# Kernel tuning notes

Measured on AMD Instinct MI355X. Metric: run time of the kernel, lower is better.

The kernel has to match this reference:

```python
import jax, jax.numpy as jnp
import numpy as np

B, L, E, H, D = 4, 4096, 1024, 16, 64  # batch, seq, embed, heads, head_dim
EPS = 1e-6


def setup_inputs() -> dict:
    key = jax.random.key(0)
    k1, k2, k3 = jax.random.split(key, 3)
    return {
        "q": jax.random.normal(k1, (B, L, E), dtype=jnp.float32),
        "k": jax.random.normal(k2, (B, L, E), dtype=jnp.float32),
        "v": jax.random.normal(k3, (B, L, E), dtype=jnp.float32),
        "mask": jnp.ones((B, L), dtype=jnp.float32),
    }


def _split_heads(x):
    # (B, L, E) -> (B*H, L, D)
    return x.reshape(B, L, H, D).transpose(0, 2, 1, 3).reshape(B * H, L, D)


def reference(q, k, v, mask):
    # feature map: relu
    q = jax.nn.relu(q)
    k = jax.nn.relu(k)
    # padding mask applied to keys/values
    k = k * mask[:, :, None]
    v = v * mask[:, :, None]
    q = _split_heads(q)
    k = _split_heads(k)
    v = _split_heads(v)
    # cosFormer sin/cos reweighting: pi/2 * i / m for i = 1..L
    idx = (np.pi / 2) * jnp.arange(1, L + 1, dtype=jnp.float32) / L
    s = jnp.sin(idx)[None, :, None]  # (1, L, 1)
    c = jnp.cos(idx)[None, :, None]
    q_ = jnp.concatenate([q * s, q * c], axis=-1)  # (B*H, L, 2D)
    k_ = jnp.concatenate([k * s, k * c], axis=-1)
    # linear-attention KV accumulation (non-causal): (B*H, 2D, D)
    kv = jnp.einsum('nld,nlm->ndm', k_, v)
    # normalizer
    z = 1.0 / jnp.maximum(jnp.einsum('nld,nd->nl', q_, k_.sum(axis=1)), EPS)
    out = jnp.einsum('nld,ndm,nl->nlm', q_, kv, z)  # (B*H, L, D)
    return out.reshape(B, H, L, D)
```

## Files before the change

### kernel.cpp

```cpp
#include <hip/hip_runtime.h>
#include <hip/hip_bf16.h>

#define B_ 4
#define L_ 4096
#define E_ 1024
#define H_ 16
#define D_ 64
#define N_ 64
#define D2_ 128
#define EPS_ 1e-6f

#define CH_ 16
#define LC_ 256
#define ANGSC (0.5f * 3.14159265358979f / (float)L_)

typedef short short8 __attribute__((ext_vector_type(8)));
typedef float f32x4 __attribute__((ext_vector_type(4)));
typedef unsigned int u32;
typedef unsigned short u16;

static __device__ __forceinline__ u16 bf16u(float x) {
  union { __hip_bfloat16 h; u16 s; } u;
  u.h = __float2bfloat16(x);
  return u.s;
}
static __device__ __forceinline__ u32 pack2bf(float a, float b) {
  return (u32)bf16u(a) | ((u32)bf16u(b) << 16);
}

__global__ __launch_bounds__(256, 4) void phase1_mfma(
    const float* __restrict__ k, const float* __restrict__ v,
    const float* __restrict__ mask,
    float* __restrict__ part_kv, float* __restrict__ part_ks) {
  __shared__ __align__(16) u16 ka[D2_ * 72];
  __shared__ __align__(16) u16 vt[D_ * 72];
  __shared__ float mm[LC_], ms[LC_], mc[LC_];

  const int bid = blockIdx.x;
  const int n = bid & 63, ch = bid >> 6;
  const int b = n >> 4, h = n & 15;
  const int t = threadIdx.x;
  const int wv = t >> 6, lane = t & 63;
  const int c_lo = lane & 15, lp = lane >> 4;
  const int c = wv * 16 + c_lo;

  {
    const int gl = ch * LC_ + t;
    const float m = mask[b * L_ + gl];
    const float ang = (float)(gl + 1) * ANGSC;
    mm[t] = m;
    ms[t] = m * __sinf(ang);
    mc[t] = m * __cosf(ang);
  }

  const float* kbase = k + (size_t)(b * L_ + ch * LC_) * E_ + h * 64 + c;
  const float* vbase = v + (size_t)(b * L_ + ch * LC_) * E_ + h * 64 + c;

  float pk0[8], pk1[8], pv0[8], pv1[8];
#pragma unroll
  for (int i = 0; i < 8; ++i) {
    const int l = 8 * i + 2 * lp;
    pk0[i] = kbase[(size_t)l * E_];
    pk1[i] = kbase[(size_t)(l + 1) * E_];
    pv0[i] = vbase[(size_t)l * E_];
    pv1[i] = vbase[(size_t)(l + 1) * E_];
  }

  f32x4 acc[2][4];
#pragma unroll
  for (int i = 0; i < 2; ++i)
#pragma unroll
    for (int j = 0; j < 4; ++j) acc[i][j] = (f32x4)0.f;
  float kss = 0.f, ksc = 0.f;

  for (int st = 0; st < 4; ++st) {
    __syncthreads();
#pragma unroll
    for (int i = 0; i < 8; ++i) {
      const int l = 8 * i + 2 * lp, lg = st * 64 + l, li = 4 * i + lp;
      const float kr0 = fmaxf(pk0[i], 0.f), kr1 = fmaxf(pk1[i], 0.f);
      const float a0 = kr0 * ms[lg], a1 = kr1 * ms[lg + 1];
      const float c0 = kr0 * mc[lg], c1 = kr1 * mc[lg + 1];
      ((u32*)ka)[c * 36 + li] = pack2bf(a0, a1);
      ((u32*)ka)[(c + 64) * 36 + li] = pack2bf(c0, c1);
      ((u32*)vt)[c * 36 + li] = pack2bf(pv0[i] * mm[lg], pv1[i] * mm[lg + 1]);
      kss += a0 + a1;
      ksc += c0 + c1;
    }
    __syncthreads();
    if (st < 3) {
      const int lo = (st + 1) * 64;
#pragma unroll
      for (int i = 0; i < 8; ++i) {
        const int l = lo + 8 * i + 2 * lp;
        pk0[i] = kbase[(size_t)l * E_];
        pk1[i] = kbase[(size_t)(l + 1) * E_];
        pv0[i] = vbase[(size_t)l * E_];
        pv1[i] = vbase[(size_t)(l + 1) * E_];
      }
    }
#pragma unroll
    for (int kk = 0; kk < 2; ++kk) {
      const int colo = kk * 32 + lp * 8;
      short8 af[2], bfr[4];
#pragma unroll
      for (int dt = 0; dt < 2; ++dt)
        af[dt] = *(const short8*)&ka[(wv * 32 + dt * 16 + c_lo) * 72 + colo];
#pragma unroll
      for (int mt = 0; mt < 4; ++mt)
        bfr[mt] = *(const short8*)&vt[(mt * 16 + c_lo) * 72 + colo];
#pragma unroll
      for (int dt = 0; dt < 2; ++dt)
#pragma unroll
        for (int mt = 0; mt < 4; ++mt)
          acc[dt][mt] = __builtin_amdgcn_mfma_f32_16x16x32_bf16(
              af[dt], bfr[mt], acc[dt][mt], 0, 0, 0);
    }
  }

  const size_t pbase = (size_t)(ch * N_ + n) * (D2_ * D_);
#pragma unroll
  for (int dt = 0; dt < 2; ++dt) {
    const int d = wv * 32 + dt * 16 + lp * 4;
#pragma unroll
    for (int mt = 0; mt < 4; ++mt) {
      const int mcol = mt * 16 + c_lo;
#pragma unroll
      for (int r = 0; r < 4; ++r)
        part_kv[pbase + (size_t)(d + r) * D_ + mcol] = acc[dt][mt][r];
    }
  }
  kss += __shfl_xor(kss, 16); kss += __shfl_xor(kss, 32);
  ksc += __shfl_xor(ksc, 16); ksc += __shfl_xor(ksc, 32);
  if (lp == 0) {
    part_ks[(size_t)(ch * N_ + n) * D2_ + c] = kss;
    part_ks[(size_t)(ch * N_ + n) * D2_ + c + 64] = ksc;
  }
}

__global__ __launch_bounds__(256) void reduce_t(
    const float* __restrict__ part_kv, const float* __restrict__ part_ks,
    u16* __restrict__ kvt, u16* __restrict__ ksb) {
  __shared__ float l0[8][65], l1[8][65];
  const int n = blockIdx.x & 63, fs = blockIdx.x >> 6;
  const int t = threadIdx.x;

#pragma unroll
  for (int p = 0; p < 4; ++p) {
    const int idx = t + 256 * p;
    const int g = idx >> 9, dd = (idx >> 6) & 7, m = idx & 63;
    const int d = g * 64 + fs * 8 + dd;
    float s = 0.f;
#pragma unroll
    for (int cc = 0; cc < CH_; ++cc)
      s += part_kv[(size_t)(cc * N_ + n) * (D2_ * D_) + d * 64 + m];
    if (g == 0) l0[dd][m] = s; else l1[dd][m] = s;
  }
  if (fs == 0 && t < D2_) {
    float s = 0.f;
#pragma unroll
    for (int cc = 0; cc < CH_; ++cc)
      s += part_ks[(size_t)(cc * N_ + n) * D2_ + t];
    const int dloc = t & 63, half = t >> 6;
    ksb[n * D2_ + 2 * dloc + half] = bf16u(s);
  }
  __syncthreads();
  u32* kvt32 = (u32*)(kvt + (size_t)n * (D_ * D2_));
#pragma unroll
  for (int p = 0; p < 2; ++p) {
    const int idx = t + 256 * p;
    const int j = idx & 7, m = idx >> 3;
    kvt32[m * 64 + fs * 8 + j] = pack2bf(l0[j][m], l1[j][m]);
  }
}

__global__ __launch_bounds__(256, 4) void phase2_mfma(
    const float* __restrict__ q, const u16* __restrict__ kvt,
    const u16* __restrict__ ksb, float* __restrict__ out) {
  const int bid = blockIdx.x;
  const int n = bid & 63, lt = bid >> 6;
  const int b = n >> 4, h = n & 15;
  const int t = threadIdx.x;
  const int wv = t >> 6, lane = t & 63;
  const int c_lo = lane & 15, quad = lane >> 4;
  const int l = lt * 64 + wv * 16 + c_lo;

  const float ang = (float)(l + 1) * ANGSC;
  const float sn = __sinf(ang), cs = __cosf(ang);

  const float* qrow = q + (size_t)(b * L_ + l) * E_ + h * 64;
  short8 af[4];
#pragma unroll
  for (int kk = 0; kk < 4; ++kk) {
    const float4 qv = *(const float4*)(qrow + kk * 16 + quad * 4);
    const float x = fmaxf(qv.x, 0.f), y = fmaxf(qv.y, 0.f);
    const float z2 = fmaxf(qv.z, 0.f), w = fmaxf(qv.w, 0.f);
    short8 a;
    a[0] = (short)bf16u(x * sn); a[1] = (short)bf16u(x * cs);
    a[2] = (short)bf16u(y * sn); a[3] = (short)bf16u(y * cs);
    a[4] = (short)bf16u(z2 * sn); a[5] = (short)bf16u(z2 * cs);
    a[6] = (short)bf16u(w * sn); a[7] = (short)bf16u(w * cs);
    af[kk] = a;
  }

  const u16* kvh = kvt + (size_t)n * (D_ * D2_);
  const u16* ksh = ksb + n * D2_;
  f32x4 acc[4], acc5 = (f32x4)0.f;
#pragma unroll
  for (int mt = 0; mt < 4; ++mt) acc[mt] = (f32x4)0.f;

#pragma unroll
  for (int kk = 0; kk < 4; ++kk) {
    const int fo = kk * 32 + quad * 8;
#pragma unroll
    for (int mt = 0; mt < 4; ++mt) {
      const short8 bfr = *(const short8*)&kvh[(mt * 16 + c_lo) * D2_ + fo];
      acc[mt] = __builtin_amdgcn_mfma_f32_16x16x32_bf16(af[kk], bfr, acc[mt], 0, 0, 0);
    }
    const short8 bks = *(const short8*)&ksh[fo];
    acc5 = __builtin_amdgcn_mfma_f32_16x16x32_bf16(af[kk], bks, acc5, 0, 0, 0);
  }

#pragma unroll
  for (int r = 0; r < 4; ++r) {
    const float den = __shfl(acc5[r], quad * 16);
    const float zz = 1.f / fmaxf(den, EPS_);
    const int gl = lt * 64 + wv * 16 + quad * 4 + r;
    float* ob = out + (size_t)n * (L_ * D_) + (size_t)gl * D_;
#pragma unroll
    for (int mt = 0; mt < 4; ++mt) ob[mt * 16 + c_lo] = acc[mt][r] * zz;
  }
}

extern "C" void kernel_launch(void* const* d_in, const int* in_sizes, int n_in,
                              void* d_out, int out_size, void* d_ws,
                              size_t ws_size, hipStream_t stream) {
  const float* q = (const float*)d_in[0];
  const float* k = (const float*)d_in[1];
  const float* v = (const float*)d_in[2];
  const float* mask = (const float*)d_in[3];
  float* out = (float*)d_out;

  float* part_kv = (float*)d_ws;
  float* part_ks = part_kv + (size_t)CH_ * N_ * D2_ * D_;
  u16* kvt = (u16*)(part_ks + (size_t)CH_ * N_ * D2_);
  u16* ksb = kvt + (size_t)N_ * D2_ * D_;

  phase1_mfma<<<dim3(CH_ * N_), dim3(256), 0, stream>>>(k, v, mask, part_kv, part_ks);
  reduce_t<<<dim3(8 * N_), dim3(256), 0, stream>>>(part_kv, part_ks, kvt, ksb);
  phase2_mfma<<<dim3(N_ * 64), dim3(256), 0, stream>>>(q, kvt, ksb, out);
}
```

Before: 266.1 us.

## Pre-transpose K/V/Q into bf16 head-major layouts before MFMA phases

Adds transpose kernels that read K, V and Q with coalesced row loads and write bf16, head-major, MFMA-friendly tiles. The sin/cos weights are moved from K onto V, and the key-sum is computed via MFMA against sin/cos tables. A single-block-per-head reduction replaces the strided reduce. The goal is to remove uncoalesced strided fp32 loads in the phase kernels, at the cost of extra launches and roughly 100MB of extra intermediate global traffic. If the workspace is too small, the old path is used instead.

```diff
diff --git a/kernel.cpp b/kernel.cpp
--- a/kernel.cpp
+++ b/kernel.cpp
@@ -9,9 +9,7 @@
 #define N_ 64
 #define D2_ 128
 #define EPS_ 1e-6f
-
 #define CH_ 16
-#define LC_ 256
 #define ANGSC (0.5f * 3.14159265358979f / (float)L_)
 
 typedef short short8 __attribute__((ext_vector_type(8)));
@@ -28,14 +26,256 @@
   return (u32)bf16u(a) | ((u32)bf16u(b) << 16);
 }
 
-__global__ __launch_bounds__(256, 4) void phase1_mfma(
+
+__global__ __launch_bounds__(256, 2) void t_kv(
+    const float* __restrict__ k, const float* __restrict__ v,
+    const float* __restrict__ mask, u32* __restrict__ kt,
+    u32* __restrict__ vs, u32* __restrict__ vc,
+    u16* __restrict__ tabs_s, u16* __restrict__ tabs_c) {
+  __shared__ float sh[16][1028];
+  __shared__ float msk[16], mss[16], msc[16];
+
+  const int bid = blockIdx.x;
+  const int b = bid >> 8, lt = bid & 255;
+  const int l0 = lt * 16;
+  const int t = threadIdx.x;
+
+  if (t < 16) {
+    const int gl = l0 + t;
+    const float m = mask[b * L_ + gl];
+    const float ang = (float)(gl + 1) * ANGSC;
+    const float s = __sinf(ang), c = __cosf(ang);
+    msk[t] = m; mss[t] = m * s; msc[t] = m * c;
+    if (b == 0) { tabs_s[gl] = bf16u(s); tabs_c[gl] = bf16u(c); }
+  }
+  __syncthreads();
+
+  {
+    const float* kb = k + (size_t)(b * L_ + l0) * E_;
+#pragma unroll
+    for (int rr = 0; rr < 4; ++rr) {
+      const int row = (t >> 6) + rr * 4;
+#pragma unroll
+      for (int seg = 0; seg < 4; ++seg) {
+        const int c4 = (t & 63) + seg * 64;
+        *(float4*)&sh[row][c4 * 4] = *(const float4*)(kb + (size_t)row * E_ + c4 * 4);
+      }
+    }
+  }
+  __syncthreads();
+  {
+    const int d = t >> 2, lw = (t & 3) * 2;
+#pragma unroll
+    for (int h = 0; h < 16; ++h) {
+      const int c = h * 64 + d;
+      const int la = 2 * lw;
+      const float x0 = fmaxf(sh[la][c], 0.f) * msk[la];
+      const float x1 = fmaxf(sh[la + 1][c], 0.f) * msk[la + 1];
+      const float x2 = fmaxf(sh[la + 2][c], 0.f) * msk[la + 2];
+      const float x3 = fmaxf(sh[la + 3][c], 0.f) * msk[la + 3];
+      const size_t base = ((size_t)(b * 16 + h) * 256 + lt) * 512;
+      uint2 val = { pack2bf(x0, x1), pack2bf(x2, x3) };
+      *(uint2*)&kt[base + d * 8 + lw] = val;
+    }
+  }
+  __syncthreads();
+  {
+    const float* vb = v + (size_t)(b * L_ + l0) * E_;
+#pragma unroll
+    for (int rr = 0; rr < 4; ++rr) {
+      const int row = (t >> 6) + rr * 4;
+#pragma unroll
+      for (int seg = 0; seg < 4; ++seg) {
+        const int c4 = (t & 63) + seg * 64;
+        *(float4*)&sh[row][c4 * 4] = *(const float4*)(vb + (size_t)row * E_ + c4 * 4);
+      }
+    }
+  }
+  __syncthreads();
+  {
+    const int m = t >> 2, lw = (t & 3) * 2;
+#pragma unroll
+    for (int h = 0; h < 16; ++h) {
+      const int c = h * 64 + m;
+      const int la = 2 * lw;
+      const float y0 = sh[la][c], y1 = sh[la + 1][c];
+      const float y2 = sh[la + 2][c], y3 = sh[la + 3][c];
+      const size_t base = ((size_t)(b * 16 + h) * 256 + lt) * 512;
+      uint2 a = { pack2bf(y0 * mss[la], y1 * mss[la + 1]),
+                  pack2bf(y2 * mss[la + 2], y3 * mss[la + 3]) };
+      uint2 cc = { pack2bf(y0 * msc[la], y1 * msc[la + 1]),
+                   pack2bf(y2 * msc[la + 2], y3 * msc[la + 3]) };
+      *(uint2*)&vs[base + m * 8 + lw] = a;
+      *(uint2*)&vc[base + m * 8 + lw] = cc;
+    }
+  }
+}
+
+__global__ __launch_bounds__(256, 4) void t_q(
+    const float* __restrict__ q, u32* __restrict__ qo) {
+  const int bid = blockIdx.x;
+  const int b = bid >> 8, l0 = (bid & 255) * 16;
+  const int t = threadIdx.x;
+  const int h = t & 15, lr = t >> 4;
+  const int l = l0 + lr;
+
+  const float ang = (float)(l + 1) * ANGSC;
+  const float s = __sinf(ang), c = __cosf(ang);
+
+  const float* qrow = q + (size_t)(b * L_ + l) * E_ + h * 64;
+  u32* qout = qo + ((size_t)(b * 16 + h) * L_ + l) * 64;
+#pragma unroll
+  for (int i = 0; i < 16; ++i) {
+    const float4 qv = *(const float4*)(qrow + i * 4);
+    const float x = fmaxf(qv.x, 0.f), y = fmaxf(qv.y, 0.f);
+    const float zz = fmaxf(qv.z, 0.f), w = fmaxf(qv.w, 0.f);
+    uint4 o = { pack2bf(x * s, x * c), pack2bf(y * s, y * c),
+                pack2bf(zz * s, zz * c), pack2bf(w * s, w * c) };
+    *(uint4*)&qout[i * 4] = o;
+  }
+}
+
+__global__ __launch_bounds__(256, 4) void p1(
+    const u16* __restrict__ kt, const u16* __restrict__ vs,
+    const u16* __restrict__ vc, const u16* __restrict__ tabs_s,
+    const u16* __restrict__ tabs_c,
+    float* __restrict__ part_kv, float* __restrict__ part_ks) {
+  const int bid = blockIdx.x;
+  const int n = bid & 63, ch = bid >> 6;
+  const int t = threadIdx.x;
+  const int wv = t >> 6, lane = t & 63;
+  const int c_lo = lane & 15, quad = lane >> 4;
+
+  const u16* ktn = kt + (size_t)n * (256 * 1024);
+  const u16* vsn = vs + (size_t)n * (256 * 1024);
+  const u16* vcn = vc + (size_t)n * (256 * 1024);
+
+  f32x4 accE[4], accO[4], aS = (f32x4)0.f, aC = (f32x4)0.f;
+#pragma unroll
+  for (int i = 0; i < 4; ++i) { accE[i] = (f32x4)0.f; accO[i] = (f32x4)0.f; }
+
+  const int d = wv * 16 + c_lo;
+#pragma unroll
+  for (int ks = 0; ks < 8; ++ks) {
+    const int lg = ch * 256 + ks * 32 + quad * 8;
+    const int ltt = lg >> 4, lin = lg & 15;
+    const short8 af = *(const short8*)&ktn[((size_t)ltt * 64 + d) * 16 + lin];
+    const short8 bs = *(const short8*)&tabs_s[lg];
+    const short8 bc = *(const short8*)&tabs_c[lg];
+    aS = __builtin_amdgcn_mfma_f32_16x16x32_bf16(af, bs, aS, 0, 0, 0);
+    aC = __builtin_amdgcn_mfma_f32_16x16x32_bf16(af, bc, aC, 0, 0, 0);
+#pragma unroll
+    for (int mt = 0; mt < 4; ++mt) {
+      const int m = mt * 16 + c_lo;
+      const short8 bE = *(const short8*)&vsn[((size_t)ltt * 64 + m) * 16 + lin];
+      const short8 bO = *(const short8*)&vcn[((size_t)ltt * 64 + m) * 16 + lin];
+      accE[mt] = __builtin_amdgcn_mfma_f32_16x16x32_bf16(af, bE, accE[mt], 0, 0, 0);
+      accO[mt] = __builtin_amdgcn_mfma_f32_16x16x32_bf16(af, bO, accO[mt], 0, 0, 0);
+    }
+  }
+
+  float* pb = part_kv + ((size_t)(ch * 64 + n)) * (128 * 64);
+#pragma unroll
+  for (int r = 0; r < 4; ++r) {
+    const int dd = wv * 16 + quad * 4 + r;
+#pragma unroll
+    for (int mt = 0; mt < 4; ++mt) {
+      const int m = mt * 16 + c_lo;
+      pb[(size_t)(2 * dd) * 64 + m] = accE[mt][r];
+      pb[(size_t)(2 * dd + 1) * 64 + m] = accO[mt][r];
+    }
+    if (c_lo == 0) {
+      part_ks[((size_t)(ch * 64 + n)) * 128 + 2 * dd] = aS[r];
+      part_ks[((size_t)(ch * 64 + n)) * 128 + 2 * dd + 1] = aC[r];
+    }
+  }
+}
+
+__global__ __launch_bounds__(256) void reduce_k(
+    const float* __restrict__ part_kv, const float* __restrict__ part_ks,
+    u16* __restrict__ kvt, u16* __restrict__ ksb) {
+  __shared__ u16 kvsh[64 * 136];
+  const int n = blockIdx.x;
+  const int t = threadIdx.x;
+
+  float a[32];
+#pragma unroll
+  for (int j = 0; j < 32; ++j) a[j] = 0.f;
+#pragma unroll
+  for (int cc = 0; cc < CH_; ++cc) {
+    const float* p = part_kv + ((size_t)(cc * 64 + n)) * 8192 + t * 32;
+#pragma unroll
+    for (int j = 0; j < 8; ++j) {
+      const float4 x = *(const float4*)(p + j * 4);
+      a[4 * j] += x.x; a[4 * j + 1] += x.y; a[4 * j + 2] += x.z; a[4 * j + 3] += x.w;
+    }
+  }
+  if (t < 128) {
+    float s = 0.f;
+#pragma unroll
+    for (int cc = 0; cc < CH_; ++cc)
+      s += part_ks[((size_t)(cc * 64 + n)) * 128 + t];
+    ksb[n * 128 + t] = bf16u(s);
+  }
+  const int f = t >> 1, m0 = (t & 1) * 32;
+#pragma unroll
+  for (int j = 0; j < 32; ++j) kvsh[(m0 + j) * 136 + f] = bf16u(a[j]);
+  __syncthreads();
+  const int m = t >> 2, fo = (t & 3) * 32;
+  u16* o = kvt + (size_t)n * 8192 + m * 128 + fo;
+#pragma unroll
+  for (int j = 0; j < 4; ++j)
+    *(short8*)(o + j * 8) = *(short8*)&kvsh[m * 136 + fo + j * 8];
+}
+
+__global__ __launch_bounds__(256, 4) void p2(
+    const u16* __restrict__ qo, const u16* __restrict__ kvt,
+    const u16* __restrict__ ksb, float* __restrict__ out) {
+  const int bid = blockIdx.x;
+  const int n = bid & 63, lt = bid >> 6;
+  const int t = threadIdx.x;
+  const int wv = t >> 6, lane = t & 63;
+  const int c_lo = lane & 15, quad = lane >> 4;
+  const int l = lt * 64 + wv * 16 + c_lo;
+
+  const u16* qrow = qo + ((size_t)n * L_ + l) * 128;
+  const u16* kvh = kvt + (size_t)n * 8192;
+  const u16* ksh = ksb + n * 128;
+
+  f32x4 acc[4], acc5 = (f32x4)0.f;
+#pragma unroll
+  for (int mt = 0; mt < 4; ++mt) acc[mt] = (f32x4)0.f;
+
+#pragma unroll
+  for (int kk = 0; kk < 4; ++kk) {
+    const int fo = kk * 32 + quad * 8;
+    const short8 af = *(const short8*)&qrow[fo];
+#pragma unroll
+    for (int mt = 0; mt < 4; ++mt) {
+      const short8 bfr = *(const short8*)&kvh[(mt * 16 + c_lo) * 128 + fo];
+      acc[mt] = __builtin_amdgcn_mfma_f32_16x16x32_bf16(af, bfr, acc[mt], 0, 0, 0);
+    }
+    const short8 bks = *(const short8*)&ksh[fo];
+    acc5 = __builtin_amdgcn_mfma_f32_16x16x32_bf16(af, bks, acc5, 0, 0, 0);
+  }
+
+#pragma unroll
+  for (int r = 0; r < 4; ++r) {
+    const float zz = 1.f / fmaxf(acc5[r], EPS_);
+    const int gl = lt * 64 + wv * 16 + quad * 4 + r;
+    float* ob = out + (size_t)n * (L_ * D_) + (size_t)gl * D_;
+#pragma unroll
+    for (int mt = 0; mt < 4; ++mt) ob[mt * 16 + c_lo] = acc[mt][r] * zz;
+  }
+}
+
+__global__ __launch_bounds__(256, 4) void r3_phase1(
     const float* __restrict__ k, const float* __restrict__ v,
     const float* __restrict__ mask,
     float* __restrict__ part_kv, float* __restrict__ part_ks) {
   __shared__ __align__(16) u16 ka[D2_ * 72];
   __shared__ __align__(16) u16 vt[D_ * 72];
-  __shared__ float mm[LC_], ms[LC_], mc[LC_];
-
+  __shared__ float mm[256], ms[256], mc[256];
   const int bid = blockIdx.x;
   const int n = bid & 63, ch = bid >> 6;
   const int b = n >> 4, h = n & 15;
@@ -43,36 +283,27 @@
   const int wv = t >> 6, lane = t & 63;
   const int c_lo = lane & 15, lp = lane >> 4;
   const int c = wv * 16 + c_lo;
-
   {
-    const int gl = ch * LC_ + t;
+    const int gl = ch * 256 + t;
     const float m = mask[b * L_ + gl];
     const float ang = (float)(gl + 1) * ANGSC;
-    mm[t] = m;
-    ms[t] = m * __sinf(ang);
-    mc[t] = m * __cosf(ang);
-  }
-
-  const float* kbase = k + (size_t)(b * L_ + ch * LC_) * E_ + h * 64 + c;
-  const float* vbase = v + (size_t)(b * L_ + ch * LC_) * E_ + h * 64 + c;
-
+    mm[t] = m; ms[t] = m * __sinf(ang); mc[t] = m * __cosf(ang);
+  }
+  const float* kbase = k + (size_t)(b * L_ + ch * 256) * E_ + h * 64 + c;
+  const float* vbase = v + (size_t)(b * L_ + ch * 256) * E_ + h * 64 + c;
   float pk0[8], pk1[8], pv0[8], pv1[8];
 #pragma unroll
   for (int i = 0; i < 8; ++i) {
     const int l = 8 * i + 2 * lp;
-    pk0[i] = kbase[(size_t)l * E_];
-    pk1[i] = kbase[(size_t)(l + 1) * E_];
-    pv0[i] = vbase[(size_t)l * E_];
-    pv1[i] = vbase[(size_t)(l + 1) * E_];
-  }
-
+    pk0[i] = kbase[(size_t)l * E_]; pk1[i] = kbase[(size_t)(l + 1) * E_];
+    pv0[i] = vbase[(size_t)l * E_]; pv1[i] = vbase[(size_t)(l + 1) * E_];
+  }
   f32x4 acc[2][4];
 #pragma unroll
   for (int i = 0; i < 2; ++i)
 #pragma unroll
     for (int j = 0; j < 4; ++j) acc[i][j] = (f32x4)0.f;
   float kss = 0.f, ksc = 0.f;
-
   for (int st = 0; st < 4; ++st) {
     __syncthreads();
 #pragma unroll
@@ -84,8 +315,7 @@
       ((u32*)ka)[c * 36 + li] = pack2bf(a0, a1);
       ((u32*)ka)[(c + 64) * 36 + li] = pack2bf(c0, c1);
       ((u32*)vt)[c * 36 + li] = pack2bf(pv0[i] * mm[lg], pv1[i] * mm[lg + 1]);
-      kss += a0 + a1;
-      ksc += c0 + c1;
+      kss += a0 + a1; ksc += c0 + c1;
     }
     __syncthreads();
     if (st < 3) {
@@ -93,10 +323,8 @@
 #pragma unroll
       for (int i = 0; i < 8; ++i) {
         const int l = lo + 8 * i + 2 * lp;
-        pk0[i] = kbase[(size_t)l * E_];
-        pk1[i] = kbase[(size_t)(l + 1) * E_];
-        pv0[i] = vbase[(size_t)l * E_];
-        pv1[i] = vbase[(size_t)(l + 1) * E_];
+        pk0[i] = kbase[(size_t)l * E_]; pk1[i] = kbase[(size_t)(l + 1) * E_];
+        pv0[i] = vbase[(size_t)l * E_]; pv1[i] = vbase[(size_t)(l + 1) * E_];
       }
     }
 #pragma unroll
@@ -117,17 +345,16 @@
               af[dt], bfr[mt], acc[dt][mt], 0, 0, 0);
     }
   }
-
   const size_t pbase = (size_t)(ch * N_ + n) * (D2_ * D_);
 #pragma unroll
   for (int dt = 0; dt < 2; ++dt) {
-    const int d = wv * 32 + dt * 16 + lp * 4;
+    const int dd = wv * 32 + dt * 16 + lp * 4;
 #pragma unroll
     for (int mt = 0; mt < 4; ++mt) {
       const int mcol = mt * 16 + c_lo;
 #pragma unroll
       for (int r = 0; r < 4; ++r)
-        part_kv[pbase + (size_t)(d + r) * D_ + mcol] = acc[dt][mt][r];
+        part_kv[pbase + (size_t)(dd + r) * D_ + mcol] = acc[dt][mt][r];
     }
   }
   kss += __shfl_xor(kss, 16); kss += __shfl_xor(kss, 32);
@@ -138,13 +365,12 @@
   }
 }
 
-__global__ __launch_bounds__(256) void reduce_t(
+__global__ __launch_bounds__(256) void r3_reduce(
     const float* __restrict__ part_kv, const float* __restrict__ part_ks,
     u16* __restrict__ kvt, u16* __restrict__ ksb) {
-  __shared__ float l0[8][65], l1[8][65];
+  __shared__ float l0s[8][65], l1s[8][65];
   const int n = blockIdx.x & 63, fs = blockIdx.x >> 6;
   const int t = threadIdx.x;
-
 #pragma unroll
   for (int p = 0; p < 4; ++p) {
     const int idx = t + 256 * p;
@@ -154,15 +380,14 @@
 #pragma unroll
     for (int cc = 0; cc < CH_; ++cc)
       s += part_kv[(size_t)(cc * N_ + n) * (D2_ * D_) + d * 64 + m];
-    if (g == 0) l0[dd][m] = s; else l1[dd][m] = s;
+    if (g == 0) l0s[dd][m] = s; else l1s[dd][m] = s;
   }
   if (fs == 0 && t < D2_) {
     float s = 0.f;
 #pragma unroll
     for (int cc = 0; cc < CH_; ++cc)
       s += part_ks[(size_t)(cc * N_ + n) * D2_ + t];
-    const int dloc = t & 63, half = t >> 6;
-    ksb[n * D2_ + 2 * dloc + half] = bf16u(s);
+    ksb[n * D2_ + 2 * (t & 63) + (t >> 6)] = bf16u(s);
   }
   __syncthreads();
   u32* kvt32 = (u32*)(kvt + (size_t)n * (D_ * D2_));
@@ -170,11 +395,11 @@
   for (int p = 0; p < 2; ++p) {
     const int idx = t + 256 * p;
     const int j = idx & 7, m = idx >> 3;
-    kvt32[m * 64 + fs * 8 + j] = pack2bf(l0[j][m], l1[j][m]);
-  }
-}
-
-__global__ __launch_bounds__(256, 4) void phase2_mfma(
+    kvt32[m * 64 + fs * 8 + j] = pack2bf(l0s[j][m], l1s[j][m]);
+  }
+}
+
+__global__ __launch_bounds__(256, 4) void r3_phase2(
     const float* __restrict__ q, const u16* __restrict__ kvt,
     const u16* __restrict__ ksb, float* __restrict__ out) {
   const int bid = blockIdx.x;
@@ -184,10 +409,8 @@
   const int wv = t >> 6, lane = t & 63;
   const int c_lo = lane & 15, quad = lane >> 4;
   const int l = lt * 64 + wv * 16 + c_lo;
-
   const float ang = (float)(l + 1) * ANGSC;
   const float sn = __sinf(ang), cs = __cosf(ang);
-
   const float* qrow = q + (size_t)(b * L_ + l) * E_ + h * 64;
   short8 af[4];
 #pragma unroll
@@ -202,13 +425,11 @@
     a[6] = (short)bf16u(w * sn); a[7] = (short)bf16u(w * cs);
     af[kk] = a;
   }
-
   const u16* kvh = kvt + (size_t)n * (D_ * D2_);
   const u16* ksh = ksb + n * D2_;
   f32x4 acc[4], acc5 = (f32x4)0.f;
 #pragma unroll
   for (int mt = 0; mt < 4; ++mt) acc[mt] = (f32x4)0.f;
-
 #pragma unroll
   for (int kk = 0; kk < 4; ++kk) {
     const int fo = kk * 32 + quad * 8;
@@ -220,7 +441,6 @@
     const short8 bks = *(const short8*)&ksh[fo];
     acc5 = __builtin_amdgcn_mfma_f32_16x16x32_bf16(af[kk], bks, acc5, 0, 0, 0);
   }
-
 #pragma unroll
   for (int r = 0; r < 4; ++r) {
     const float den = __shfl(acc5[r], quad * 16);
@@ -240,13 +460,43 @@
   const float* v = (const float*)d_in[2];
   const float* mask = (const float*)d_in[3];
   float* out = (float*)d_out;
-
-  float* part_kv = (float*)d_ws;
-  float* part_ks = part_kv + (size_t)CH_ * N_ * D2_ * D_;
-  u16* kvt = (u16*)(part_ks + (size_t)CH_ * N_ * D2_);
-  u16* ksb = kvt + (size_t)N_ * D2_ * D_;
-
-  phase1_mfma<<<dim3(CH_ * N_), dim3(256), 0, stream>>>(k, v, mask, part_kv, part_ks);
-  reduce_t<<<dim3(8 * N_), dim3(256), 0, stream>>>(part_kv, part_ks, kvt, ksb);
-  phase2_mfma<<<dim3(N_ * 64), dim3(256), 0, stream>>>(q, kvt, ksb, out);
-}
+  char* ws = (char*)d_ws;
+
+  const size_t SZ_KT = 33554432, SZ_VS = 33554432, SZ_VC = 33554432;
+  const size_t SZ_PKV = 33554432, SZ_PKS = 524288, SZ_KVT = 1048576;
+  const size_t SZ_KSB = 16384, SZ_TAB = 16384;
+  const size_t o_kt = 0, o_vs = o_kt + SZ_KT, o_vc = o_vs + SZ_VS;
+  const size_t o_pkv = o_vc + SZ_VC, o_pks = o_pkv + SZ_PKV;
+  const size_t o_kvt = o_pks + SZ_PKS, o_ksb = o_kvt + SZ_KVT;
+  const size_t o_ts = o_ksb + SZ_KSB, o_tc = o_ts + SZ_TAB / 2;
+  const size_t need = o_tc + SZ_TAB / 2;
+
+  if (ws_size >= need) {
+    u32* kt = (u32*)(ws + o_kt);
+    u32* vs = (u32*)(ws + o_vs);
+    u32* vc = (u32*)(ws + o_vc);
+    float* part_kv = (float*)(ws + o_pkv);
+    float* part_ks = (float*)(ws + o_pks);
+    u16* kvt = (u16*)(ws + o_kvt);
+    u16* ksb = (u16*)(ws + o_ksb);
+    u16* tabs_s = (u16*)(ws + o_ts);
+    u16* tabs_c = (u16*)(ws + o_tc);
+    u32* qo = (u32*)(ws + o_kt);
+
+    t_kv<<<dim3(4 * 256), dim3(256), 0, stream>>>(k, v, mask, kt, vs, vc,
+                                                  tabs_s, tabs_c);
+    p1<<<dim3(CH_ * 64), dim3(256), 0, stream>>>((u16*)kt, (u16*)vs, (u16*)vc,
+                                                 tabs_s, tabs_c, part_kv, part_ks);
+    t_q<<<dim3(4 * 256), dim3(256), 0, stream>>>(q, qo);
+    reduce_k<<<dim3(64), dim3(256), 0, stream>>>(part_kv, part_ks, kvt, ksb);
+    p2<<<dim3(64 * 64), dim3(256), 0, stream>>>((u16*)qo, kvt, ksb, out);
+  } else {
+    float* part_kv = (float*)d_ws;
+    float* part_ks = part_kv + (size_t)CH_ * N_ * D2_ * D_;
+    u16* kvt = (u16*)(part_ks + (size_t)CH_ * N_ * D2_);
+    u16* ksb = kvt + (size_t)N_ * D2_ * D_;
+    r3_phase1<<<dim3(CH_ * N_), dim3(256), 0, stream>>>(k, v, mask, part_kv, part_ks);
+    r3_reduce<<<dim3(8 * N_), dim3(256), 0, stream>>>(part_kv, part_ks, kvt, ksb);
+    r3_phase2<<<dim3(N_ * 64), dim3(256), 0, stream>>>(q, kvt, ksb, out);
+  }
+}
```

Result: slower. 343.1 us (+28.9%).
